# Optimization experiments

Hardware: AMD Instinct MI355X
Metric: run time of the kernel (lower is better)

## Reference

```python
import jax, jax.numpy as jnp
import numpy as np

NUM_CLASSES = 60
K = 512
D = 256
B, H, W = 32, 64, 64


def setup_inputs() -> dict:
    key = jax.random.key(0)
    k1, k2, k3 = jax.random.split(key, 3)
    z_e_x = jax.random.normal(k1, (B, D, H, W), dtype=jnp.float32)
    c = jax.random.randint(k2, (B,), 0, NUM_CLASSES)
    embedding = jax.random.normal(k3, (NUM_CLASSES * K, D), dtype=jnp.float32) * 0.02
    return {"z_e_x": z_e_x, "c": c, "embedding": embedding}


def reference(z_e_x, c, embedding):
    # z_e_x: [B, D, H, W], c: [B] int class labels, embedding: [num_classes*K, D]
    b, d, h, w = z_e_x.shape
    z = jnp.transpose(z_e_x, (0, 2, 3, 1)).reshape(b, h * w, d)  # [B, N, D]
    # Per-batch class-specific codebook slice: equivalent to the torch loop over
    # classes with embedding.weight[key*K:(key+1)*K], vectorized over batch.
    cb = embedding.reshape(NUM_CLASSES, K, d)[c]  # [B, K, D]
    # Squared euclidean distances (cdist^2): ||z||^2 - 2 z.cb^T + ||cb||^2
    z_sq = jnp.sum(z * z, axis=-1, keepdims=True)          # [B, N, 1]
    cb_sq = jnp.sum(cb * cb, axis=-1)[:, None, :]          # [B, 1, K]
    dots = jnp.einsum('bnd,bkd->bnk', z, cb)               # [B, N, K]
    dist = z_sq - 2.0 * dots + cb_sq                       # [B, N, K]
    idx = jnp.argmin(dist, axis=-1)                        # [B, N]
    quantized = jnp.take_along_axis(cb, idx[..., None], axis=1)  # [B, N, D]
    return quantized.reshape(b, h, w, d)  # [B, H, W, D], matches latents layout
```

## Files before the change

kernel.cpp:

```cpp
#include <hip/hip_runtime.h>
#include <cstdint>

#define NCLS 60
#define KC 512
#define DD 256
#define BB 32
#define NP 4096
#define LDP 260
#define EPS 1e-2f
#define PER_CLS 2048
#define ZBLOCKS (BB * (NP / 64))
#define CBLOCKS ((NCLS * KC) / 64)

typedef _Float16 f16;
typedef _Float16 f16x8 __attribute__((ext_vector_type(8)));
typedef float f32x4 __attribute__((ext_vector_type(4)));
typedef float v2f __attribute__((ext_vector_type(2)));
typedef unsigned long long u64;

__device__ __forceinline__ float mul_rn_nofuse(float a, float b) {
  float p = a * b;
  asm("" : "+v"(p));
  return p;
}

__device__ __forceinline__ v2f pk_mul(v2f a, v2f b) {
  v2f d;
  asm("v_pk_mul_f32 %0, %1, %2" : "=v"(d) : "v"(a), "v"(b));
  return d;
}
__device__ __forceinline__ v2f pk_add(v2f a, v2f b) {
  v2f d;
  asm("v_pk_add_f32 %0, %1, %2" : "=v"(d) : "v"(a), "v"(b));
  return d;
}

__device__ __forceinline__ float np_pairwise128_sq(const float* a) {
  float r[8];
#pragma unroll
  for (int j = 0; j < 8; ++j) r[j] = mul_rn_nofuse(a[j], a[j]);
  for (int blk = 1; blk < 16; ++blk) {
#pragma unroll
    for (int j = 0; j < 8; ++j) {
      float p = mul_rn_nofuse(a[blk * 8 + j], a[blk * 8 + j]);
      r[j] = r[j] + p;
    }
  }
  return ((r[0] + r[1]) + (r[2] + r[3])) + ((r[4] + r[5]) + (r[6] + r[7]));
}

__global__ __launch_bounds__(256) void vq_prep_kernel(
    const float* __restrict__ z, const float* __restrict__ emb,
    float* __restrict__ zsq, float* __restrict__ cbsq,
    f16* __restrict__ zT_h, f16* __restrict__ cb_h) {
  __shared__ float buf[64][LDP];
  __shared__ float half2[64][2];
  const int t = threadIdx.x;

  if (blockIdx.x < ZBLOCKS) {
    const int b = blockIdx.x >> 6;
    const int n0 = (blockIdx.x & 63) * 64;
    const float* zb = z + (size_t)b * DD * NP;
    const int n = t & 63, dq = t >> 6;
#pragma unroll 4
    for (int it = 0; it < 64; ++it) {
      int d = it * 4 + dq;
      buf[n][d] = zb[(size_t)d * NP + n0 + n];
    }
    __syncthreads();
    f16* ob = zT_h + ((size_t)b * NP + n0) * DD;
#pragma unroll
    for (int it = 0; it < 16; ++it) {
      int row = it * 4 + dq;
      union { f16 h[4]; uint2 u; } pk;
#pragma unroll
      for (int j = 0; j < 4; ++j) pk.h[j] = (f16)buf[row][n * 4 + j];
      *(uint2*)&ob[(size_t)row * DD + n * 4] = pk.u;
    }
    if (t < 128) {
      int r = t & 63, h = t >> 6;
      half2[r][h] = np_pairwise128_sq(&buf[r][h * 128]);
    }
    __syncthreads();
    if (t < 64) zsq[b * NP + n0 + t] = half2[t][0] + half2[t][1];
  } else {
    const int r0 = (blockIdx.x - ZBLOCKS) * 64;
    const float4* e4 = (const float4*)emb;
#pragma unroll
    for (int i = 0; i < 16; ++i) {
      int flat = i * 256 + t;
      int row = flat >> 6, col4 = flat & 63;
      *(float4*)&buf[row][col4 * 4] = e4[(size_t)(r0 + row) * 64 + col4];
    }
    __syncthreads();
    if (t < 128) {
      int r = t & 63, h = t >> 6;
      half2[r][h] = np_pairwise128_sq(&buf[r][h * 128]);
    }
#pragma unroll
    for (int i = 0; i < 16; ++i) {
      int flat = i * 256 + t;
      int row = flat >> 6, q4 = flat & 63;
      union { f16 h[4]; uint2 u; } pk;
#pragma unroll
      for (int j = 0; j < 4; ++j) pk.h[j] = (f16)buf[row][q4 * 4 + j];
      *(uint2*)&cb_h[(size_t)(r0 + row) * DD + q4 * 4] = pk.u;
    }
    __syncthreads();
    if (t < 64) cbsq[r0 + t] = half2[t][0] + half2[t][1];
  }
}

__global__ __launch_bounds__(256) void vq_mfma_kernel(
    const f16* __restrict__ zT_h, const int* __restrict__ c,
    const f16* __restrict__ cb_h, const float* __restrict__ cbsq,
    int* __restrict__ idx_out, unsigned int* __restrict__ counters,
    unsigned int* __restrict__ lists) {
  __shared__ __align__(16) f16 zs[64][264];
  __shared__ __align__(16) f16 cs[128][72];
  const int t = threadIdx.x;
  const int id = blockIdx.x;
  const int xcd = id & 7;
  const int j = id >> 3;
  const int b = xcd * 4 + (j >> 6);
  const int n0 = (j & 63) * 64;
  const int wave = t >> 6;
  const int wm = wave >> 1, wn = wave & 1;
  const int l = t & 63, lr = l & 15, lg = l >> 4;
  const int cls = c[b];
  const f16* __restrict__ zTb = zT_h + ((size_t)b * NP + n0) * DD;
  const f16* __restrict__ cbb = cb_h + (size_t)cls * KC * DD;
  const float* __restrict__ cbsqb = cbsq + cls * KC;
  const int crow0 = t >> 3, cseg = (t & 7) * 8;

#define LOADC(q)                                                               \
  do {                                                                         \
    const int kn_ = (q) >> 2, dn_ = (q) & 3;                                   \
    const f16* p_ = cbb + ((size_t)(kn_ * 128 + crow0)) * DD + dn_ * 64 + cseg;\
    rc0 = *(const f16x8*)(p_);                                                 \
    rc1 = *(const f16x8*)(p_ + (size_t)32 * DD);                               \
    rc2 = *(const f16x8*)(p_ + (size_t)64 * DD);                               \
    rc3 = *(const f16x8*)(p_ + (size_t)96 * DD);                               \
  } while (0)

#define WRITEC()                                                               \
  do {                                                                         \
    *(f16x8*)&cs[crow0][cseg] = rc0;                                           \
    *(f16x8*)&cs[crow0 + 32][cseg] = rc1;                                      \
    *(f16x8*)&cs[crow0 + 64][cseg] = rc2;                                      \
    *(f16x8*)&cs[crow0 + 96][cseg] = rc3;                                      \
  } while (0)

#pragma unroll
  for (int i = 0; i < 8; ++i) {
    int flat = i * 256 + t;
    int row = flat >> 5, seg = flat & 31;
    *(f16x8*)&zs[row][seg * 8] = *(const f16x8*)&zTb[(size_t)row * DD + seg * 8];
  }

  float m1[8], m2[8];
  int i1[8];
#pragma unroll
  for (int r = 0; r < 8; ++r) { m1[r] = 3.4e38f; m2[r] = 3.4e38f; i1[r] = 0; }

  f32x4 acc[2][4];
#pragma unroll
  for (int mi = 0; mi < 2; ++mi)
#pragma unroll
    for (int nj = 0; nj < 4; ++nj) acc[mi][nj] = (f32x4){0.f, 0.f, 0.f, 0.f};

  f16x8 rc0, rc1, rc2, rc3;
  LOADC(0);
  __syncthreads();
  WRITEC();
  __syncthreads();

#pragma unroll 1
  for (int p = 0; p < 16; ++p) {
    if (p < 15) LOADC(p + 1);
    const int dzb = (p & 3) * 64;
#pragma unroll
    for (int s = 0; s < 2; ++s) {
      const int dz = dzb + s * 32 + lg * 8;
      const int dcs = s * 32 + lg * 8;
      f16x8 af[2], bf[4];
#pragma unroll
      for (int mi = 0; mi < 2; ++mi)
        af[mi] = *(const f16x8*)&zs[wm * 32 + mi * 16 + lr][dz];
#pragma unroll
      for (int nj = 0; nj < 4; ++nj)
        bf[nj] = *(const f16x8*)&cs[wn * 64 + nj * 16 + lr][dcs];
#pragma unroll
      for (int mi = 0; mi < 2; ++mi)
#pragma unroll
        for (int nj = 0; nj < 4; ++nj)
          acc[mi][nj] = __builtin_amdgcn_mfma_f32_16x16x32_f16(
              af[mi], bf[nj], acc[mi][nj], 0, 0, 0);
    }
    if ((p & 3) == 3) {
      const int kt = p >> 2;
#pragma unroll
      for (int nj = 0; nj < 4; ++nj) {
        const int k = kt * 128 + wn * 64 + nj * 16 + lr;
        const float cq = cbsqb[k];
#pragma unroll
        for (int mi = 0; mi < 2; ++mi)
#pragma unroll
          for (int rg = 0; rg < 4; ++rg) {
            const int ri = mi * 4 + rg;
            float dist = fmaf(-2.0f, acc[mi][nj][rg], cq);
            if (dist < m1[ri]) {
              m2[ri] = m1[ri]; m1[ri] = dist; i1[ri] = k;
            } else if (dist < m2[ri]) {
              m2[ri] = dist;
            }
          }
      }
#pragma unroll
      for (int mi = 0; mi < 2; ++mi)
#pragma unroll
        for (int nj = 0; nj < 4; ++nj) acc[mi][nj] = (f32x4){0.f, 0.f, 0.f, 0.f};
    }
    __syncthreads();
    if (p < 15) {
      WRITEC();
      __syncthreads();
    }
  }

#pragma unroll
  for (int r = 0; r < 8; ++r) {
#pragma unroll
    for (int off = 8; off >= 1; off >>= 1) {
      float om1 = __shfl_xor(m1[r], off);
      float om2 = __shfl_xor(m2[r], off);
      int oi = __shfl_xor(i1[r], off);
      bool take = (om1 < m1[r]) || (om1 == m1[r] && oi < i1[r]);
      if (take) {
        m2[r] = fminf(m1[r], om2);
        m1[r] = om1;
        i1[r] = oi;
      } else {
        m2[r] = fminf(m2[r], om1);
      }
    }
  }

  float* redm = (float*)&zs[0][0];
  int* redi = (int*)&cs[0][0];
  if (lr == 0) {
#pragma unroll
    for (int r = 0; r < 8; ++r) {
      int row = wm * 32 + (r >> 2) * 16 + lg * 4 + (r & 3);
      redm[(wn * 64 + row) * 2 + 0] = m1[r];
      redm[(wn * 64 + row) * 2 + 1] = m2[r];
      redi[wn * 64 + row] = i1[r];
    }
  }
  __syncthreads();
  if (t < 64) {
    const int row = t;
    float a1 = redm[row * 2], a2 = redm[row * 2 + 1];
    int ai = redi[row];
    float b1 = redm[(64 + row) * 2], b2 = redm[(64 + row) * 2 + 1];
    int bi2 = redi[64 + row];
    float f1, f2;
    int idx;
    if (b1 < a1) { f1 = b1; idx = bi2; f2 = fminf(a1, b2); }
    else { f1 = a1; idx = ai; f2 = fminf(b1, a2); }
    const int n = n0 + row;
    idx_out[b * NP + n] = idx;
    if (f2 - f1 < EPS) {
      unsigned p = atomicAdd(&counters[cls], 1u);
      if (p < PER_CLS) lists[cls * PER_CLS + p] = ((unsigned)b << 12) | (unsigned)n;
    }
  }
#undef LOADC
#undef WRITEC
}

__global__ __launch_bounds__(256) void vq_fix_kernel(
    const float* __restrict__ z, const float* __restrict__ emb,
    const float* __restrict__ zsq, const float* __restrict__ cbsq,
    u64* __restrict__ best_g, const unsigned int* __restrict__ counters,
    const unsigned int* __restrict__ lists) {
  const int cls = blockIdx.x;
  unsigned cnt = counters[cls];
  if (cnt > PER_CLS) cnt = PER_CLS;
  const int grp = blockIdx.y >> 3;
  const int kz = blockIdx.y & 7;
  const unsigned base = grp * 32;
  if (base >= cnt) return;
  const int t = threadIdx.x;

  __shared__ float zrow[32][LDP];
  __shared__ float cbt[32][LDP];
  __shared__ float zq[32];
  __shared__ unsigned bn[32];
  __shared__ float red_v[256];
  __shared__ int red_k[256];

  if (t < 32) {
    unsigned p = base + t;
    unsigned e = (p < cnt) ? lists[cls * PER_CLS + p] : 0xFFFFFFFFu;
    bn[t] = e;
    zq[t] = (e != 0xFFFFFFFFu) ? zsq[(e >> 12) * NP + (e & (NP - 1))] : 0.f;
  }
  __syncthreads();
  {
    int r = t >> 3, d0 = t & 7;
    unsigned e = bn[r];
    if (e != 0xFFFFFFFFu) {
      int bb = (int)(e >> 12), nn = (int)(e & (NP - 1));
      const float* zp = z + (size_t)bb * DD * NP + nn;
#pragma unroll
      for (int j = 0; j < 32; ++j) zrow[r][d0 + j * 8] = zp[(size_t)(d0 + j * 8) * NP];
    }
  }

  const int pg = t & 15;
  const int kg = t >> 4;
  const bool val0 = (bn[pg] != 0xFFFFFFFFu);
  const bool val1 = (bn[pg + 16] != 0xFFFFFFFFu);
  float best[2] = {3.4e38f, 3.4e38f};
  int bk[2] = {0x7FFFFFFF, 0x7FFFFFFF};

#pragma unroll 1
  for (int tt = 0; tt < 2; ++tt) {
    const int tile = kz * 2 + tt;
    __syncthreads();
#pragma unroll
    for (int j = 0; j < 8; ++j) {
      int flat = j * 256 + t;
      int row = flat >> 6, col4 = flat & 63;
      *(float4*)&cbt[row][col4 * 4] =
          *(const float4*)&emb[((size_t)cls * KC + tile * 32 + row) * DD + col4 * 4];
    }
    __syncthreads();

    v2f A2[2][2][2];
#pragma unroll
    for (int ps = 0; ps < 2; ++ps)
#pragma unroll
      for (int ks = 0; ks < 2; ++ks) {
        A2[ps][ks][0] = (v2f){0.f, 0.f};
        A2[ps][ks][1] = (v2f){0.f, 0.f};
      }

#pragma unroll 1
    for (int c16 = 0; c16 < 16; ++c16) {
      v2f za2[2][8], ca2[2][8];
#pragma unroll
      for (int q = 0; q < 4; ++q) {
        float4 z0 = *(const float4*)&zrow[pg][c16 * 16 + q * 4];
        float4 z1 = *(const float4*)&zrow[pg + 16][c16 * 16 + q * 4];
        float4 c0 = *(const float4*)&cbt[kg][c16 * 16 + q * 4];
        float4 c1 = *(const float4*)&cbt[kg + 16][c16 * 16 + q * 4];
        za2[0][q * 2 + 0] = (v2f){z0.x, z0.y};
        za2[0][q * 2 + 1] = (v2f){z0.z, z0.w};
        za2[1][q * 2 + 0] = (v2f){z1.x, z1.y};
        za2[1][q * 2 + 1] = (v2f){z1.z, z1.w};
        ca2[0][q * 2 + 0] = (v2f){c0.x, c0.y};
        ca2[0][q * 2 + 1] = (v2f){c0.z, c0.w};
        ca2[1][q * 2 + 0] = (v2f){c1.x, c1.y};
        ca2[1][q * 2 + 1] = (v2f){c1.z, c1.w};
      }
#pragma unroll
      for (int s = 3; s >= 0; --s)
#pragma unroll
        for (int ps = 0; ps < 2; ++ps)
#pragma unroll
          for (int ks = 0; ks < 2; ++ks) {
            A2[ps][ks][0] =
                pk_add(pk_mul(za2[ps][s * 2 + 0], ca2[ks][s * 2 + 0]), A2[ps][ks][0]);
            A2[ps][ks][1] =
                pk_add(pk_mul(za2[ps][s * 2 + 1], ca2[ks][s * 2 + 1]), A2[ps][ks][1]);
          }
    }

#pragma unroll
    for (int ps = 0; ps < 2; ++ps) {
      const float zqv = zq[pg + 16 * ps];
#pragma unroll
      for (int ks = 0; ks < 2; ++ks) {
        const int k = tile * 32 + kg + 16 * ks;
        float dot = (A2[ps][ks][0].x + A2[ps][ks][0].y) +
                    (A2[ps][ks][1].x + A2[ps][ks][1].y);
        float dist = (zqv - 2.0f * dot) + cbsq[cls * KC + k];
        if (dist < best[ps]) { best[ps] = dist; bk[ps] = k; }
      }
    }
  }

#pragma unroll
  for (int s = 0; s < 2; ++s) {
    __syncthreads();
    red_v[t] = best[s];
    red_k[t] = bk[s];
    __syncthreads();
    for (int off = 8; off >= 1; off >>= 1) {
      if (kg < off) {
        int o = t + 16 * off;
        float ov = red_v[o];
        int ok = red_k[o];
        if (ov < red_v[t] || (ov == red_v[t] && ok < red_k[t])) {
          red_v[t] = ov;
          red_k[t] = ok;
        }
      }
      __syncthreads();
    }
    if (kg == 0 && ((s == 0 && val0) || (s == 1 && val1))) {
      unsigned e = bn[pg + 16 * s];
      unsigned u = __float_as_uint(red_v[t]);
      u = (u & 0x80000000u) ? ~u : (u | 0x80000000u);
      u64 pkd = ((u64)u << 32) | (unsigned)red_k[t];
      atomicMin(&best_g[(e >> 12) * NP + (e & (NP - 1))], pkd);
    }
  }
}

__global__ __launch_bounds__(256) void vq_commit_kernel(
    const u64* __restrict__ best_g, const unsigned int* __restrict__ counters,
    const unsigned int* __restrict__ lists, int* __restrict__ idx_out) {
  const int cls = blockIdx.x;
  unsigned cnt = counters[cls];
  if (cnt > PER_CLS) cnt = PER_CLS;
  for (unsigned i = threadIdx.x; i < cnt; i += 256) {
    unsigned e = lists[cls * PER_CLS + i];
    int pos = (int)(e >> 12) * NP + (int)(e & (NP - 1));
    u64 v = best_g[pos];
    if (v != ~0ull) idx_out[pos] = (int)(unsigned)(v & 0xFFFFFFFFu);
  }
}

__global__ __launch_bounds__(256) void vq_gather_kernel(
    const int* __restrict__ c, const float* __restrict__ emb,
    const int* __restrict__ idx, float* __restrict__ out) {
  int t = threadIdx.x;
  int r = blockIdx.x * 4 + (t >> 6);
  int lane = t & 63;
  int b = r >> 12;
  int k = idx[r];
  const float4* src = (const float4*)(emb + (size_t)(c[b] * KC + k) * DD);
  float4* dst = (float4*)(out + (size_t)r * DD);
  dst[lane] = src[lane];
}

extern "C" void kernel_launch(void* const* d_in, const int* in_sizes, int n_in,
                              void* d_out, int out_size, void* d_ws, size_t ws_size,
                              hipStream_t stream) {
  const float* z = (const float*)d_in[0];
  const int* c = (const int*)d_in[1];
  const float* emb = (const float*)d_in[2];
  float* out = (float*)d_out;

  char* ws = (char*)d_ws;
  float* zsq = (float*)ws;
  float* cbsq = (float*)(ws + 524288);
  int* idx = (int*)(ws + 655360);
  unsigned int* counters = (unsigned int*)(ws + 1179648);
  unsigned int* lists = (unsigned int*)(ws + 1179904);

  f16* zT_h = (f16*)d_out;
  f16* cb_h = (f16*)((char*)d_out + (size_t)BB * NP * DD * 2);
  u64* best_g = (u64*)((char*)d_out + 82837504);

  hipMemsetAsync(counters, 0, NCLS * sizeof(unsigned int), stream);
  hipMemsetAsync(best_g, 0xFF, (size_t)BB * NP * 8, stream);
  vq_prep_kernel<<<ZBLOCKS + CBLOCKS, 256, 0, stream>>>(z, emb, zsq, cbsq, zT_h, cb_h);
  vq_mfma_kernel<<<ZBLOCKS, 256, 0, stream>>>(zT_h, c, cb_h, cbsq, idx, counters, lists);
  dim3 gF(NCLS, (PER_CLS / 32) * 8);
  vq_fix_kernel<<<gF, 256, 0, stream>>>(z, emb, zsq, cbsq, best_g, counters, lists);
  vq_commit_kernel<<<NCLS, 256, 0, stream>>>(best_g, counters, lists, idx);
  vq_gather_kernel<<<(BB * NP) / 4, 256, 0, stream>>>(c, emb, idx, out);
}
```

Before: 318.7 us.

## Keep z tile in registers and double-buffer codebook LDS tiles

Each wave now loads its z fragments from global memory straight into registers instead of staging the 64x256 z tile in shared memory. The freed LDS holds a two-slot codebook buffer, so the next slice is written into the other slot and each step needs one barrier instead of two. This removes the z LDS traffic and cuts synchronisation in the MFMA loop. The cost is about 64 extra VGPRs per thread for the z fragments, which may reduce occupancy.

```diff
diff --git a/kernel.cpp b/kernel.cpp
--- a/kernel.cpp
+++ b/kernel.cpp
@@ -116,8 +116,7 @@
     const f16* __restrict__ cb_h, const float* __restrict__ cbsq,
     int* __restrict__ idx_out, unsigned int* __restrict__ counters,
     unsigned int* __restrict__ lists) {
-  __shared__ __align__(16) f16 zs[64][264];
-  __shared__ __align__(16) f16 cs[128][72];
+  __shared__ __align__(16) f16 cs[2][128][72];
   const int t = threadIdx.x;
   const int id = blockIdx.x;
   const int xcd = id & 7;
@@ -143,19 +142,20 @@
     rc3 = *(const f16x8*)(p_ + (size_t)96 * DD);                               \
   } while (0)
 
-#define WRITEC()                                                               \
+#define WRITEC(B)                                                              \
   do {                                                                         \
-    *(f16x8*)&cs[crow0][cseg] = rc0;                                           \
-    *(f16x8*)&cs[crow0 + 32][cseg] = rc1;                                      \
-    *(f16x8*)&cs[crow0 + 64][cseg] = rc2;                                      \
-    *(f16x8*)&cs[crow0 + 96][cseg] = rc3;                                      \
+    *(f16x8*)&cs[B][crow0][cseg] = rc0;                                        \
+    *(f16x8*)&cs[B][crow0 + 32][cseg] = rc1;                                   \
+    *(f16x8*)&cs[B][crow0 + 64][cseg] = rc2;                                   \
+    *(f16x8*)&cs[B][crow0 + 96][cseg] = rc3;                                   \
   } while (0)
 
-#pragma unroll
-  for (int i = 0; i < 8; ++i) {
-    int flat = i * 256 + t;
-    int row = flat >> 5, seg = flat & 31;
-    *(f16x8*)&zs[row][seg * 8] = *(const f16x8*)&zTb[(size_t)row * DD + seg * 8];
+  f16x8 zf[2][8];
+#pragma unroll
+  for (int mi = 0; mi < 2; ++mi) {
+    const f16* zr = zTb + (size_t)(wm * 32 + mi * 16 + lr) * DD + lg * 8;
+#pragma unroll
+    for (int ks = 0; ks < 8; ++ks) zf[mi][ks] = *(const f16x8*)(zr + ks * 32);
   }
 
   float m1[8], m2[8];
@@ -171,59 +171,55 @@
 
   f16x8 rc0, rc1, rc2, rc3;
   LOADC(0);
+  WRITEC(0);
   __syncthreads();
-  WRITEC();
-  __syncthreads();
 
 #pragma unroll 1
-  for (int p = 0; p < 16; ++p) {
-    if (p < 15) LOADC(p + 1);
-    const int dzb = (p & 3) * 64;
-#pragma unroll
-    for (int s = 0; s < 2; ++s) {
-      const int dz = dzb + s * 32 + lg * 8;
-      const int dcs = s * 32 + lg * 8;
-      f16x8 af[2], bf[4];
-#pragma unroll
-      for (int mi = 0; mi < 2; ++mi)
-        af[mi] = *(const f16x8*)&zs[wm * 32 + mi * 16 + lr][dz];
-#pragma unroll
-      for (int nj = 0; nj < 4; ++nj)
-        bf[nj] = *(const f16x8*)&cs[wn * 64 + nj * 16 + lr][dcs];
-#pragma unroll
-      for (int mi = 0; mi < 2; ++mi)
+  for (int kt = 0; kt < 4; ++kt) {
+#pragma unroll
+    for (int dc = 0; dc < 4; ++dc) {
+      const int q = kt * 4 + dc;
+      const int buf = dc & 1;
+      if (kt < 3 || dc < 3) LOADC(q + 1);
+#pragma unroll
+      for (int s = 0; s < 2; ++s) {
+        const int dcs = s * 32 + lg * 8;
+        f16x8 bf[4];
 #pragma unroll
         for (int nj = 0; nj < 4; ++nj)
-          acc[mi][nj] = __builtin_amdgcn_mfma_f32_16x16x32_f16(
-              af[mi], bf[nj], acc[mi][nj], 0, 0, 0);
-    }
-    if ((p & 3) == 3) {
-      const int kt = p >> 2;
-#pragma unroll
-      for (int nj = 0; nj < 4; ++nj) {
-        const int k = kt * 128 + wn * 64 + nj * 16 + lr;
-        const float cq = cbsqb[k];
+          bf[nj] = *(const f16x8*)&cs[buf][wn * 64 + nj * 16 + lr][dcs];
 #pragma unroll
         for (int mi = 0; mi < 2; ++mi)
 #pragma unroll
-          for (int rg = 0; rg < 4; ++rg) {
-            const int ri = mi * 4 + rg;
-            float dist = fmaf(-2.0f, acc[mi][nj][rg], cq);
-            if (dist < m1[ri]) {
-              m2[ri] = m1[ri]; m1[ri] = dist; i1[ri] = k;
-            } else if (dist < m2[ri]) {
-              m2[ri] = dist;
+          for (int nj = 0; nj < 4; ++nj)
+            acc[mi][nj] = __builtin_amdgcn_mfma_f32_16x16x32_f16(
+                zf[mi][dc * 2 + s], bf[nj], acc[mi][nj], 0, 0, 0);
+      }
+      if (dc == 3) {
+#pragma unroll
+        for (int nj = 0; nj < 4; ++nj) {
+          const int k = kt * 128 + wn * 64 + nj * 16 + lr;
+          const float cq = cbsqb[k];
+#pragma unroll
+          for (int mi = 0; mi < 2; ++mi)
+#pragma unroll
+            for (int rg = 0; rg < 4; ++rg) {
+              const int ri = mi * 4 + rg;
+              float dist = fmaf(-2.0f, acc[mi][nj][rg], cq);
+              if (dist < m1[ri]) {
+                m2[ri] = m1[ri]; m1[ri] = dist; i1[ri] = k;
+              } else if (dist < m2[ri]) {
+                m2[ri] = dist;
+              }
             }
-          }
-      }
-#pragma unroll
-      for (int mi = 0; mi < 2; ++mi)
-#pragma unroll
-        for (int nj = 0; nj < 4; ++nj) acc[mi][nj] = (f32x4){0.f, 0.f, 0.f, 0.f};
-    }
-    __syncthreads();
-    if (p < 15) {
-      WRITEC();
+        }
+#pragma unroll
+        for (int mi = 0; mi < 2; ++mi)
+#pragma unroll
+          for (int nj = 0; nj < 4; ++nj)
+            acc[mi][nj] = (f32x4){0.f, 0.f, 0.f, 0.f};
+      }
+      if (kt < 3 || dc < 3) WRITEC(buf ^ 1);
       __syncthreads();
     }
   }
@@ -246,8 +242,8 @@
     }
   }
 
-  float* redm = (float*)&zs[0][0];
-  int* redi = (int*)&cs[0][0];
+  float* redm = (float*)&cs[0][0][0];
+  int* redi = (int*)&cs[1][0][0];
   if (lr == 0) {
 #pragma unroll
     for (int r = 0; r < 8; ++r) {
```

Measured after the change: 310.3 us. -2.6%, faster.
